# Optimization experiments

Hardware: AMD Instinct MI355X
Metric: run time of the kernel (lower is better)

The kernel has to match this reference:

```python
import jax, jax.numpy as jnp
import numpy as np

S, B, E = 4096, 2, 1024
H = 8
WIN = 256  # one-sided window w; band width = 2*w+1


def _band_scores(q, k_pad, seq_len, band):
    # q: (B,S,H,D), k_pad: (B,S+2w,H,D). Returns (B,S,H,band) banded QK^T.
    def f(o):
        ks = jax.lax.dynamic_slice_in_dim(k_pad, o, seq_len, axis=1)
        return jnp.einsum('bshd,bshd->bsh', q, ks)
    s = jax.lax.map(f, jnp.arange(band))  # (band,B,S,H)
    return jnp.moveaxis(s, 0, -1)          # (B,S,H,band)


def _band_av(probs, v_pad, seq_len, band):
    # probs: (B,S,H,band), v_pad: (B,S+2w,H,D) zero-padded (out-of-range keys
    # contribute zero vectors, matching diagonaled_mm's internal masking).
    bsz, _, heads, _ = probs.shape
    d = v_pad.shape[-1]
    def body(carry, o):
        vs = jax.lax.dynamic_slice_in_dim(v_pad, o, seq_len, axis=1)
        p = jax.lax.dynamic_slice_in_dim(probs, o, 1, axis=3)  # (B,S,H,1)
        return carry + p * vs, None
    init = jnp.zeros((bsz, seq_len, heads, d), probs.dtype)
    out, _ = jax.lax.scan(body, init, jnp.arange(band))
    return out


def setup_inputs() -> dict:
    key = jax.random.key(0)
    ks = jax.random.split(key, 7)
    val = jax.random.normal(ks[0], (S, B, E), dtype=jnp.float32)
    Wq = jax.random.normal(ks[1], (E, E), dtype=jnp.float32) * 0.02
    bq = jax.random.normal(ks[2], (E,), dtype=jnp.float32) * 0.02
    Wk = jax.random.normal(ks[3], (E, E), dtype=jnp.float32) * 0.02
    bk = jax.random.normal(ks[4], (E,), dtype=jnp.float32) * 0.02
    Wv = jax.random.normal(ks[5], (E, E), dtype=jnp.float32) * 0.02
    bv = jax.random.normal(ks[6], (E,), dtype=jnp.float32) * 0.02
    return {"val": val, "Wq": Wq, "bq": bq, "Wk": Wk, "bk": bk, "Wv": Wv, "bv": bv}


def reference(val, Wq, bq, Wk, bk, Wv, bv):
    seq_len, bsz, embed = val.shape
    heads, w = H, WIN
    d = embed // heads
    band = 2 * w + 1
    x = jnp.swapaxes(val, 0, 1)  # (B,S,E), matches val.transpose(0,1)
    scale = 1.0 / np.sqrt(d)
    q = (x @ Wq.T + bq) * scale
    k = x @ Wk.T + bk
    v = x @ Wv.T + bv
    # Faithful to torch: .view(seq_len, bsz, H, D) on a (bsz, seq_len, E)
    # contiguous tensor reinterprets memory (a scramble when B != S), then
    # transpose(0,1). jnp.reshape on row-major matches torch .view exactly.
    mq = jnp.swapaxes(q.reshape(seq_len, bsz, heads, d), 0, 1)  # (B,S,H,D)
    mk = jnp.swapaxes(k.reshape(seq_len, bsz, heads, d), 0, 1)
    mv = jnp.swapaxes(v.reshape(seq_len, bsz, heads, d), 0, 1)
    k_pad = jnp.pad(mk, ((0, 0), (w, w), (0, 0), (0, 0)))  # zero pad => padding=0 scores
    v_pad = jnp.pad(mv, ((0, 0), (w, w), (0, 0), (0, 0)))
    scores = _band_scores(mq, k_pad, seq_len, band)  # (B,S,H,2w+1)
    # No masking before softmax (faithful: padding=0 entries enter softmax as 0)
    probs = jax.nn.softmax(scores, axis=-1)
    # dropout in eval mode (training=False) is identity
    attn = _band_av(probs, v_pad, seq_len, band)  # (B,S,H,D)
    out = jnp.swapaxes(attn, 0, 1).reshape(seq_len, bsz, embed)
    return out
```

## Files before the change

kernel.cpp:

```cpp
#include <hip/hip_runtime.h>
#include <stdint.h>

#define SEQ   4096
#define EMB   1024
#define HD    128
#define WIN   256
#define MROWS 8192

typedef unsigned short u16;
typedef unsigned long long u64;
typedef __bf16 v8bf  __attribute__((ext_vector_type(8)));
typedef float  v4f   __attribute__((ext_vector_type(4)));
typedef u16    v8u16 __attribute__((ext_vector_type(8)));
typedef short  v4ss  __attribute__((ext_vector_type(4)));

__device__ __forceinline__ void mfma16(v4f& c, v4ss a, v4ss b) {
  asm("s_nop 1\n\tv_mfma_f32_16x16x16_bf16 %0, %1, %2, %0"
      : "+v"(c) : "v"(a), "v"(b));
}

__device__ __forceinline__ u16 f2bf(float f) {
  uint32_t u = __builtin_bit_cast(uint32_t, f);
  u += 0x7FFFu + ((u >> 16) & 1u);
  return (u16)(u >> 16);
}
__device__ __forceinline__ void gl_lds16(const u16* g, u16* l) {
  __builtin_amdgcn_global_load_lds((const __attribute__((address_space(1))) void*)g,
                                   (__attribute__((address_space(3))) void*)l,
                                   16, 0, 0);
}

__global__ __launch_bounds__(256)
void cvt_f32_bf16(const float* __restrict__ val,
                  const float* __restrict__ Wq,
                  const float* __restrict__ Wk,
                  const float* __restrict__ Wv,
                  u16* __restrict__ valbf, u16* __restrict__ Wbf)
{
  const int seg = blockIdx.y;
  const float* src; u16* dst; int nblk;
  if (seg == 0)      { src = val; dst = valbf;              nblk = 4096; }
  else if (seg == 1) { src = Wq;  dst = Wbf;                nblk = 512;  }
  else if (seg == 2) { src = Wk;  dst = Wbf + (1u << 20);   nblk = 512;  }
  else               { src = Wv;  dst = Wbf + (2u << 20);   nblk = 512;  }
  if ((int)blockIdx.x >= nblk) return;
  const int t = blockIdx.x * 256 + threadIdx.x;
  float4 a = ((const float4*)src)[2 * t];
  float4 b = ((const float4*)src)[2 * t + 1];
  v8u16 o;
  o[0] = f2bf(a.x); o[1] = f2bf(a.y); o[2] = f2bf(a.z); o[3] = f2bf(a.w);
  o[4] = f2bf(b.x); o[5] = f2bf(b.y); o[6] = f2bf(b.z); o[7] = f2bf(b.w);
  ((v8u16*)dst)[t] = o;
}

__global__ __launch_bounds__(256, 3)
void qkv_gemm(const u16* __restrict__ valbf, const u16* __restrict__ Wbf,
              const float* __restrict__ bq, const float* __restrict__ bk,
              const float* __restrict__ bv,
              u16* __restrict__ Qb, u16* __restrict__ Kb, u16* __restrict__ VTg)
{
  __shared__ __align__(16) u16 As[128 * 64];
  __shared__ __align__(16) u16 Bs[128 * 64];

  const int tid  = threadIdx.x;
  const int lane = tid & 63;
  const int w    = tid >> 6;
  const int quad = lane >> 4;
  const int lq   = lane & 15;
  const int wm   = w >> 1, wn = w & 1;

  const int bm = blockIdx.x;
  const int bn = blockIdx.y;

  const int seg = bn >> 3;
  const u16*   Wsel = Wbf + (size_t)seg * EMB * EMB;
  const float* bsel = seg == 0 ? bq : (seg == 1 ? bk : bv);
  const int nseg0 = (bn & 7) * 128;

  const u16* arow[4];
  const u16* brow[4];
#pragma unroll
  for (int call = 0; call < 4; ++call) {
    int c  = call * 256 + w * 64 + lane;
    int m  = c >> 3;
    int qs = c & 7;
    int q  = qs ^ (m & 7);
    int a2 = bm * 128 + m;
    int aa = 2 * (a2 & 4095) + (a2 >> 12);
    int grow = (aa & 4095) * 2 + (aa >> 12);
    arow[call] = valbf + (size_t)grow * EMB + q * 8;
    int n = nseg0 + m;
    brow[call] = Wsel + (size_t)n * EMB + q * 8;
  }

  v4f acc[4][4];
#pragma unroll
  for (int mt = 0; mt < 4; ++mt)
#pragma unroll
    for (int nt = 0; nt < 4; ++nt) acc[mt][nt] = (v4f){0.f, 0.f, 0.f, 0.f};

#pragma unroll 1
  for (int kt = 0; kt < 16; ++kt) {
    const int k0 = kt * 64;
    __syncthreads();
#pragma unroll
    for (int call = 0; call < 4; ++call) {
      gl_lds16(arow[call] + k0, &As[(call * 256 + w * 64) * 8]);
      gl_lds16(brow[call] + k0, &Bs[(call * 256 + w * 64) * 8]);
    }
    __syncthreads();
#pragma unroll
    for (int ks = 0; ks < 2; ++ks) {
      v8bf afr[4], bfr[4];
      const int qa = ks * 4 + quad;
#pragma unroll
      for (int mt = 0; mt < 4; ++mt) {
        int m = wm * 64 + mt * 16 + lq;
        afr[mt] = *(const v8bf*)&As[(m * 8 + (qa ^ (m & 7))) * 8];
      }
#pragma unroll
      for (int nt = 0; nt < 4; ++nt) {
        int n = wn * 64 + nt * 16 + lq;
        bfr[nt] = *(const v8bf*)&Bs[(n * 8 + (qa ^ (n & 7))) * 8];
      }
#pragma unroll
      for (int mt = 0; mt < 4; ++mt)
#pragma unroll
        for (int nt = 0; nt < 4; ++nt)
          acc[mt][nt] = __builtin_amdgcn_mfma_f32_16x16x32_bf16(afr[mt], bfr[nt], acc[mt][nt], 0, 0, 0);
    }
  }

  const float scale = 0.08838834764831845f;
  float bias[4];
#pragma unroll
  for (int nt = 0; nt < 4; ++nt)
    bias[nt] = bsel[nseg0 + wn * 64 + nt * 16 + lq];

  if (seg == 2) {
    const int h  = bn & 7;
    const int bp = bm >> 5;
    const int s0 = (bm & 31) * 128;
#pragma unroll
    for (int mt = 0; mt < 4; ++mt) {
      int mb = wm * 64 + mt * 16 + quad * 4;
#pragma unroll
      for (int nt = 0; nt < 4; ++nt) {
        int n = wn * 64 + nt * 16 + lq;
        u64 pk = 0;
#pragma unroll
        for (int r = 0; r < 4; ++r)
          pk |= (u64)f2bf(acc[mt][nt][r] + bias[nt]) << (16 * r);
        *(u64*)&VTg[((size_t)(bp * 8 + h) * HD + n) * SEQ + s0 + mb] = pk;
      }
    }
  } else {
    u16* Osel = (seg == 0) ? Qb : Kb;
#pragma unroll
    for (int mt = 0; mt < 4; ++mt) {
      int rbase = bm * 128 + wm * 64 + mt * 16 + quad * 4;
#pragma unroll
      for (int nt = 0; nt < 4; ++nt) {
        int ncol = nseg0 + wn * 64 + nt * 16 + lq;
#pragma unroll
        for (int r = 0; r < 4; ++r) {
          float v = acc[mt][nt][r] + bias[nt];
          if (seg == 0) v *= scale;
          Osel[(size_t)(rbase + r) * EMB + ncol] = f2bf(v);
        }
      }
    }
  }
}

__global__ __launch_bounds__(256, 4)
void local_attn(const u16* __restrict__ Qb, const u16* __restrict__ Kb,
                const u16* __restrict__ VTg, float* __restrict__ out)
{
  __shared__ __align__(16) u16 sK [64 * 128];
  __shared__ __align__(16) u16 sVT[128 * 64];

  const int tid  = threadIdx.x;
  const int lane = tid & 63;
  const int w    = tid >> 6;
  const int quad = lane >> 4;
  const int lq   = lane & 15;

  const int bh = blockIdx.x;
  const int q0 = blockIdx.y * 64;
  const int bp = bh >> 3;
  const int h  = bh & 7;
  const size_t rowbase = (size_t)bp * SEQ;

  const u16* Kbase = Kb + rowbase * EMB + h * HD;
  const u16* Vbase = VTg + (size_t)bh * HD * SEQ;

  v8bf qf[4];
  {
    const u16* qrow = Qb + (rowbase + q0 + w * 16 + lq) * EMB + h * HD;
#pragma unroll
    for (int ks = 0; ks < 4; ++ks)
      qf[ks] = *(const v8bf*)(qrow + ks * 32 + quad * 8);
  }

  v4f oaccT[8];
#pragma unroll
  for (int dt = 0; dt < 8; ++dt) oaccT[dt] = (v4f){0.f, 0.f, 0.f, 0.f};
  float ls = 0.f;

  const int jlo = (q0 - WIN > 0) ? q0 - WIN : 0;
  const int jhi = (q0 + 64 + WIN < SEQ) ? q0 + 64 + WIN : SEQ;
  const int nit = (jhi - jlo) >> 6;

  auto stage = [&](int kb) {
#pragma unroll
    for (int call = 0; call < 4; ++call) {
      int s = call * 256 + w * 64 + lane;
      int row = s >> 4, sl = s & 15;
      int q = sl ^ (row & 15);
      gl_lds16(Kbase + (size_t)(kb + row) * EMB + q * 8,
               &sK[(call * 256 + w * 64) * 8]);
    }
#pragma unroll
    for (int call = 0; call < 4; ++call) {
      int s = call * 256 + w * 64 + lane;
      int d = s >> 3, sl = s & 7;
      int q = sl ^ (d & 7);
      gl_lds16(Vbase + (size_t)d * SEQ + kb + q * 8,
               &sVT[(call * 256 + w * 64) * 8]);
    }
  };

#pragma unroll 1
  for (int it = 0; it < nit; ++it) {
    const int kb = jlo + it * 64;
    stage(kb);
    __syncthreads();

    v4f st[4];
#pragma unroll
    for (int nt = 0; nt < 4; ++nt) st[nt] = (v4f){0.f, 0.f, 0.f, 0.f};
#pragma unroll
    for (int ks = 0; ks < 4; ++ks) {
      const int sl = (ks * 4 + quad) ^ lq;
#pragma unroll
      for (int nt = 0; nt < 4; ++nt) {
        v8bf kf = *(const v8bf*)&sK[((nt * 16 + lq) * 16 + sl) * 8];
        st[nt] = __builtin_amdgcn_mfma_f32_16x16x32_bf16(kf, qf[ks], st[nt], 0, 0, 0);
      }
    }

    const bool need_mask = (kb == q0 - 256) || (kb == q0 + 256);
    v4ss pf[4];
#pragma unroll
    for (int nt = 0; nt < 4; ++nt) {
#pragma unroll
      for (int r = 0; r < 4; ++r) {
        float pv = __expf(st[nt][r]);
        if (need_mask) {
          int j  = kb + nt * 16 + quad * 4 + r;
          int sr = q0 + w * 16 + lq;
          int dd = j - sr;
          pv = (dd <= WIN && dd >= -WIN) ? pv : 0.f;
        }
        ls += pv;
        pf[nt][r] = (short)f2bf(pv);
      }
    }

#pragma unroll
    for (int nt = 0; nt < 4; ++nt) {
#pragma unroll
      for (int dt = 0; dt < 8; ++dt) {
        int d = dt * 16 + lq;
        int slot = (nt * 2 + (quad >> 1)) ^ (d & 7);
        v4ss vt = *(const v4ss*)&sVT[(d * 8 + slot) * 8 + (quad & 1) * 4];
        mfma16(oaccT[dt], vt, pf[nt]);
      }
    }
    __syncthreads();
  }

  asm volatile("s_nop 7\n\ts_nop 7");

  {
    float t = ls;
    t += __shfl_xor(t, 16);
    t += __shfl_xor(t, 32);
    const int sr = q0 + w * 16 + lq;
    int npl = WIN - sr;             if (npl < 0) npl = 0;
    int npr = sr - (SEQ - 1 - WIN); if (npr < 0) npr = 0;
    const float inv = 1.0f / (t + (float)(npl + npr));
    float* orow = out + (size_t)(2 * sr + bp) * EMB + h * HD;
#pragma unroll
    for (int dt = 0; dt < 8; ++dt) {
      v4f o;
#pragma unroll
      for (int r = 0; r < 4; ++r) o[r] = oaccT[dt][r] * inv;
      *(v4f*)(orow + dt * 16 + quad * 4) = o;
    }
  }
}

extern "C" void kernel_launch(void* const* d_in, const int* in_sizes, int n_in,
                              void* d_out, int out_size, void* d_ws, size_t ws_size,
                              hipStream_t stream) {
  const float* val = (const float*)d_in[0];
  const float* bq  = (const float*)d_in[2];
  const float* bk  = (const float*)d_in[4];
  const float* bv  = (const float*)d_in[6];
  float* out = (float*)d_out;

  u16* valbf = (u16*)d_ws;
  u16* Wbf   = valbf + (size_t)MROWS * EMB;
  u16* Qb    = Wbf + (size_t)3 * EMB * EMB;
  u16* Kb    = Qb + (size_t)MROWS * EMB;
  u16* VTg   = Kb + (size_t)MROWS * EMB;

  hipLaunchKernelGGL(cvt_f32_bf16, dim3(4096, 4), dim3(256), 0, stream,
                     val, (const float*)d_in[1], (const float*)d_in[3],
                     (const float*)d_in[5], valbf, Wbf);
  hipLaunchKernelGGL(qkv_gemm, dim3(64, 24), dim3(256), 0, stream,
                     valbf, Wbf, bq, bk, bv, Qb, Kb, VTg);
  hipLaunchKernelGGL(local_attn, dim3(16, 64), dim3(256), 0, stream,
                     Qb, Kb, VTg, out);
}
```

Measured before the change: 187.8 us.

## Register-prefetch next K/V tile to overlap global loads with MFMA compute

Replaces the direct global-to-LDS staging of each K/V tile with a software pipeline. The next tile is loaded into registers while the current tile is computed, then written to LDS at the start of the following iteration. This is meant to hide global memory latency behind the QK and PV MFMA work. In exchange it uses 8 extra uint4 registers per thread, which can lower occupancy, and it moves the barrier to the top of the loop.

```diff
diff --git a/kernel.cpp b/kernel.cpp
--- a/kernel.cpp
+++ b/kernel.cpp
@@ -212,29 +212,40 @@
   const int jhi = (q0 + 64 + WIN < SEQ) ? q0 + 64 + WIN : SEQ;
   const int nit = (jhi - jlo) >> 6;
 
-  auto stage = [&](int kb) {
-#pragma unroll
-    for (int call = 0; call < 4; ++call) {
-      int s = call * 256 + w * 64 + lane;
-      int row = s >> 4, sl = s & 15;
+  uint4 kpf[4], vpf[4];
+  auto prefetch = [&](int kb) {
+#pragma unroll
+    for (int i = 0; i < 4; ++i) {
+      int g = w * 256 + i * 64 + lane;
+      int row = g >> 4, sl = g & 15;
       int q = sl ^ (row & 15);
-      gl_lds16(Kbase + (size_t)(kb + row) * EMB + q * 8,
-               &sK[(call * 256 + w * 64) * 8]);
-    }
-#pragma unroll
-    for (int call = 0; call < 4; ++call) {
-      int s = call * 256 + w * 64 + lane;
-      int d = s >> 3, sl = s & 7;
+      kpf[i] = *(const uint4*)(Kbase + (size_t)(kb + row) * EMB + q * 8);
+    }
+#pragma unroll
+    for (int i = 0; i < 4; ++i) {
+      int g = w * 256 + i * 64 + lane;
+      int d = g >> 3, sl = g & 7;
       int q = sl ^ (d & 7);
-      gl_lds16(Vbase + (size_t)d * SEQ + kb + q * 8,
-               &sVT[(call * 256 + w * 64) * 8]);
+      vpf[i] = *(const uint4*)(Vbase + (size_t)d * SEQ + kb + q * 8);
     }
   };
+  auto commit = [&]() {
+#pragma unroll
+    for (int i = 0; i < 4; ++i)
+      *(uint4*)&sK[(w * 256 + i * 64 + lane) * 8] = kpf[i];
+#pragma unroll
+    for (int i = 0; i < 4; ++i)
+      *(uint4*)&sVT[(w * 256 + i * 64 + lane) * 8] = vpf[i];
+  };
+
+  prefetch(jlo);
 
 #pragma unroll 1
   for (int it = 0; it < nit; ++it) {
     const int kb = jlo + it * 64;
-    stage(kb);
+    __syncthreads();
+    commit();
+    if (it + 1 < nit) prefetch(kb + 64);
     __syncthreads();
 
     v4f st[4];
@@ -278,7 +289,6 @@
         mfma16(oaccT[dt], vt, pf[nt]);
       }
     }
-    __syncthreads();
   }
 
   asm volatile("s_nop 7\n\ts_nop 7");
```

Result: slower. 280.3 us (+49.2%).
